# Optimization experiments

Hardware: AMD Instinct MI355X
Metric: run time of the kernel (lower is better)

Reference implementation:

```python
import jax, jax.numpy as jnp
import numpy as np
import math

BT, N, D, H = 16, 1024, 128, 8
HD = D // H


def setup_inputs() -> dict:
    key = jax.random.key(0)
    ks = jax.random.split(key, 12)
    s = 1.0 / math.sqrt(D)
    return {
        "x": jax.random.normal(ks[0], (BT, N, D), dtype=jnp.float32),
        "adj": jax.random.uniform(ks[1], (BT, N, N), dtype=jnp.float32),
        "Wq": jax.random.normal(ks[2], (D, D), dtype=jnp.float32) * s,
        "bq": jax.random.normal(ks[3], (D,), dtype=jnp.float32) * 0.01,
        "Wk": jax.random.normal(ks[4], (D, D), dtype=jnp.float32) * s,
        "bk": jax.random.normal(ks[5], (D,), dtype=jnp.float32) * 0.01,
        "Wv": jax.random.normal(ks[6], (D, D), dtype=jnp.float32) * s,
        "bv": jax.random.normal(ks[7], (D,), dtype=jnp.float32) * 0.01,
        "Wo": jax.random.normal(ks[8], (D, D), dtype=jnp.float32) * s,
        "bo": jax.random.normal(ks[9], (D,), dtype=jnp.float32) * 0.01,
    }


def reference(x, adj, Wq, bq, Wk, bk, Wv, bv, Wo, bo):
    bt, n, d = x.shape
    # projections (torch Linear: x @ W.T + b), split into heads -> (BT,H,N,HD)
    q = (x @ Wq.T + bq).reshape(bt, n, H, HD).transpose(0, 2, 1, 3)
    k = (x @ Wk.T + bk).reshape(bt, n, H, HD).transpose(0, 2, 1, 3)
    v = (x @ Wv.T + bv).reshape(bt, n, H, HD).transpose(0, 2, 1, 3)
    scores = jnp.einsum('bhnd,bhmd->bhnm', q, k) / math.sqrt(HD)  # (BT,H,N,N)
    mask = (adj == 0)[:, None, :, :]  # (BT,1,N,N)
    scores = jnp.where(mask, -jnp.inf, scores)
    attn = jax.nn.softmax(scores, axis=-1)
    attn = attn * adj[:, None, :, :]  # reweight by continuous causal strength
    attn = attn / (attn.sum(axis=-1, keepdims=True) + 1e-8)  # renormalize
    ctx = jnp.einsum('bhnm,bhmd->bhnd', attn, v)  # (BT,H,N,HD)
    ctx = ctx.transpose(0, 2, 1, 3).reshape(bt, n, d)
    return ctx @ Wo.T + bo
```

## Files before the change

kernel.cpp:

```cpp
#include <hip/hip_runtime.h>
#include <hip/hip_bf16.h>

#define BTC 16
#define NC 1024
#define DC 128
#define HC 8
#define HDC 16

typedef __attribute__((ext_vector_type(8))) short bf16x8;
typedef __attribute__((ext_vector_type(4))) float f32x4;
typedef __attribute__((ext_vector_type(16))) float f32x16;
typedef __attribute__((ext_vector_type(4))) short short4v;

#if __has_builtin(__builtin_amdgcn_exp2f)
#define EXP2F(x) __builtin_amdgcn_exp2f(x)
#else
#define EXP2F(x) exp2f(x)
#endif

#define QSCALE 0.36067376022224085f

union PK2 { short4v s4; __hip_bfloat162 h2[2]; };
union PK8 { bf16x8 v; short s[8]; __hip_bfloat162 h2[4]; };

static __device__ inline short f2bf(float f) {
    unsigned u = __builtin_bit_cast(unsigned, f);
    u += 0x7fffu + ((u >> 16) & 1u);
    return (short)(u >> 16);
}

#define LDS_BARRIER()                                              \
    do {                                                           \
        asm volatile("s_waitcnt lgkmcnt(0)" ::: "memory");         \
        __builtin_amdgcn_s_barrier();                              \
        asm volatile("" ::: "memory");                             \
    } while (0)

__global__ __launch_bounds__(256)
void prep_kernel(const float* __restrict__ x,
                 const float* __restrict__ Wq, const float* __restrict__ Wk,
                 const float* __restrict__ Wv, const float* __restrict__ Wo,
                 short* __restrict__ xbf, short* __restrict__ Wbf)
{
    int gid  = blockIdx.x * 256 + threadIdx.x;
    int base = gid * 4;
    const float* src;
    short* dst;
    if (base < 2097152) {
        src = x + base; dst = xbf + base;
    } else {
        int idx = base - 2097152;
        int w   = idx >> 14;
        int off = idx & 16383;
        src = ((w == 0) ? Wq : (w == 1) ? Wk : (w == 2) ? Wv : Wo) + off;
        dst = Wbf + w * 16384 + off;
    }
    float4 v = *(const float4*)src;
    PK2 pk;
    pk.h2[0] = __float22bfloat162_rn(make_float2(v.x, v.y));
    pk.h2[1] = __float22bfloat162_rn(make_float2(v.z, v.w));
    *(short4v*)dst = pk.s4;
}

__global__ __launch_bounds__(256)
void proj_qkv(const short* __restrict__ xbf, const short* __restrict__ Wbf,
              const float* __restrict__ bq, const float* __restrict__ bk,
              const float* __restrict__ bv,
              short* __restrict__ qo, short* __restrict__ ko, short* __restrict__ vto)
{
    __shared__ short T[128 * 72];

    const int y = blockIdx.y;
    const short* W = Wbf + y * 16384;
    const float* bias = (y == 0) ? bq : (y == 1) ? bk : bv;
    const float scale = (y == 0) ? QSCALE : 1.0f;

    const int tid  = threadIdx.x;
    const int wave = tid >> 6;
    const int lane = tid & 63;
    const int l15  = lane & 15;
    const int quad = lane >> 4;
    const int rowA = blockIdx.x * 64 + wave * 16;

    f32x4 acc[8];
#pragma unroll
    for (int t = 0; t < 8; ++t) acc[t] = (f32x4){0.f, 0.f, 0.f, 0.f};

#pragma unroll
    for (int kk = 0; kk < DC; kk += 32) {
        bf16x8 Af = *(const bf16x8*)&xbf[(size_t)(rowA + l15) * DC + kk + quad * 8];
#pragma unroll
        for (int t = 0; t < 8; ++t) {
            bf16x8 Bf = *(const bf16x8*)&W[(t * 16 + l15) * DC + kk + quad * 8];
            acc[t] = __builtin_amdgcn_mfma_f32_16x16x32_bf16(Af, Bf, acc[t], 0, 0, 0);
        }
    }

    if (y == 2) {
#pragma unroll
        for (int t = 0; t < 8; ++t) {
            int c = t * 16 + l15;
            float b = bias[c];
            PK2 pk;
            pk.h2[0] = __float22bfloat162_rn(make_float2(acc[t][0] + b, acc[t][1] + b));
            pk.h2[1] = __float22bfloat162_rn(make_float2(acc[t][2] + b, acc[t][3] + b));
            *(short4v*)&T[c * 72 + wave * 16 + quad * 4] = pk.s4;
        }
        __syncthreads();
        const int bt = blockIdx.x >> 4;
        const int n0 = (blockIdx.x * 64) & 1023;
        const int chunk = tid & 7;
        const int dr    = tid >> 3;
#pragma unroll
        for (int rep = 0; rep < 4; ++rep) {
            int d = rep * 32 + dr;
            bf16x8 u = *(const bf16x8*)&T[d * 72 + chunk * 8];
            *(bf16x8*)&vto[((size_t)bt * DC + d) * NC + n0 + chunk * 8] = u;
        }
    } else {
        short* dst = (y == 0) ? qo : ko;
#pragma unroll
        for (int t = 0; t < 8; ++t) {
            int c  = t * 16 + l15;
            int hh = c >> 4, dd = c & 15;
            float b = bias[c];
#pragma unroll
            for (int r = 0; r < 4; ++r) {
                int row = rowA + quad * 4 + r;
                int btq = row >> 10, n = row & 1023;
                float val = (acc[t][r] + b) * scale;
                dst[(((size_t)btq * HC + hh) * NC + n) * HDC + dd] = f2bf(val);
            }
        }
    }
}

__global__ __launch_bounds__(256)
void proj_out(const short* __restrict__ cbf, const short* __restrict__ Wobf,
              const float* __restrict__ bo, float* __restrict__ out)
{
    const int tid  = threadIdx.x;
    const int wave = tid >> 6;
    const int lane = tid & 63;
    const int l15  = lane & 15;
    const int quad = lane >> 4;
    const int rowA = blockIdx.x * 64 + wave * 16;

    f32x4 acc[8];
#pragma unroll
    for (int t = 0; t < 8; ++t) acc[t] = (f32x4){0.f, 0.f, 0.f, 0.f};

#pragma unroll
    for (int kk = 0; kk < DC; kk += 32) {
        bf16x8 Af = *(const bf16x8*)&cbf[(size_t)(rowA + l15) * DC + kk + quad * 8];
#pragma unroll
        for (int t = 0; t < 8; ++t) {
            bf16x8 Bf = *(const bf16x8*)&Wobf[(t * 16 + l15) * DC + kk + quad * 8];
            acc[t] = __builtin_amdgcn_mfma_f32_16x16x32_bf16(Af, Bf, acc[t], 0, 0, 0);
        }
    }

#pragma unroll
    for (int t = 0; t < 8; ++t) {
        int c = t * 16 + l15;
        float b = bo[c];
#pragma unroll
        for (int r = 0; r < 4; ++r) {
            int row = rowA + quad * 4 + r;
            out[(size_t)row * DC + c] = acc[t][r] + b;
        }
    }
}

__global__ __launch_bounds__(512, 4)
void attn_kernel(const short* __restrict__ qh, const short* __restrict__ kh,
                 const short* __restrict__ vt, const float* __restrict__ adj,
                 short* __restrict__ cb)
{
    __shared__ float As[2][32 * 36];
    __shared__ short Ps[8][2][32 * 40];

    const int tid  = threadIdx.x;
    const int wave = tid >> 6;
    const int lane = tid & 63;
    const int l31  = lane & 31;
    const int hi   = lane >> 5;
    const int l15  = lane & 15;
    const int quad = lane >> 4;
    const int bt   = blockIdx.y;
    const int qt0  = blockIdx.x * 32;
    const int h    = wave;

    const size_t xb = (size_t)bt * NC * DC;
    const size_t hb = ((size_t)bt * HC + h) * NC;

    const short* kp = kh + hb * HDC + hi * 8;
    const short* vp = vt + ((size_t)bt * DC + h * HDC + l15) * NC;
    const int arow = tid >> 4;
    const int acol = (tid & 15) * 2;
    const float* aptr = adj + (size_t)bt * NC * NC + (size_t)(qt0 + arow) * NC + acol;

    float2 ar  = *(const float2*)aptr;
    bf16x8 Ak  = *(const bf16x8*)&kp[(size_t)l31 * HDC];
    bf16x8 Bv  = *(const bf16x8*)&vp[quad * 8];
    const bf16x8 Bq = *(const bf16x8*)&qh[(hb + qt0 + l31) * HDC + hi * 8];

    PK8 ones;
#pragma unroll
    for (int j = 0; j < 8; ++j) ones.s[j] = (short)0x3F80;

    f32x16 Z16;
#pragma unroll
    for (int i = 0; i < 16; ++i) Z16[i] = 0.f;

    f32x4 Cc[2], Cw[2];
#pragma unroll
    for (int s = 0; s < 2; ++s) {
        Cc[s] = (f32x4){0.f, 0.f, 0.f, 0.f};
        Cw[s] = (f32x4){0.f, 0.f, 0.f, 0.f};
    }

#define EXPTILE(Sv, abuf, Pc)                                                 \
    do {                                                                      \
        _Pragma("unroll")                                                     \
        for (int t = 0; t < 4; ++t) {                                         \
            float4 a4 = *(const float4*)&As[abuf][l31 * 36 + t * 8 + hi * 4]; \
            float p0 = EXP2F(Sv[4 * t + 0]) * a4.x;                           \
            float p1 = EXP2F(Sv[4 * t + 1]) * a4.y;                           \
            float p2 = EXP2F(Sv[4 * t + 2]) * a4.z;                           \
            float p3 = EXP2F(Sv[4 * t + 3]) * a4.w;                           \
            PK2 pk;                                                           \
            pk.h2[0] = __float22bfloat162_rn(make_float2(p0, p1));            \
            pk.h2[1] = __float22bfloat162_rn(make_float2(p2, p3));            \
            *(short4v*)&Pc[l31 * 40 + t * 8 + hi * 4] = pk.s4;                \
        }                                                                     \
    } while (0)

    {
        *(float2*)&As[0][arow * 36 + acol] = ar;
        float2 arn = *(const float2*)(aptr + 32);
        LDS_BARRIER();
        bf16x8 Akn = *(const bf16x8*)&kp[(size_t)(32 + l31) * HDC];
        bf16x8 Bvn = *(const bf16x8*)&vp[32 + quad * 8];
        f32x16 S = __builtin_amdgcn_mfma_f32_32x32x16_bf16(Ak, Bq, Z16, 0, 0, 0);
        short* Pc = &Ps[wave][0][0];
        EXPTILE(S, 0, Pc);
        Ak = Akn; Bv = Bvn; ar = arn;
    }
    bf16x8 Bvp = Bv;

    Bvp = *(const bf16x8*)&vp[quad * 8];

#pragma unroll 2
    for (int it = 1; it < 32; ++it) {
        const int jt  = it * 32;
        const int cur = it & 1, prv = cur ^ 1;

        *(float2*)&As[cur][arow * 36 + acol] = ar;
        float2 arn = *(const float2*)(aptr + ((jt + 32) & (NC - 1)));
        LDS_BARRIER();

        const int nj = (jt + 32) & (NC - 1);
        bf16x8 Akn = *(const bf16x8*)&kp[(size_t)(nj + l31) * HDC];
        bf16x8 Bvn = *(const bf16x8*)&vp[nj + quad * 8];

        const short* Pr = &Ps[wave][prv][0];
        bf16x8 Ap0 = *(const bf16x8*)&Pr[l15 * 40 + quad * 8];
        bf16x8 Ap1 = *(const bf16x8*)&Pr[(16 + l15) * 40 + quad * 8];

        f32x16 S = __builtin_amdgcn_mfma_f32_32x32x16_bf16(Ak, Bq, Z16, 0, 0, 0);
        short* Pc = &Ps[wave][cur][0];
        EXPTILE(S, cur, Pc);

        __builtin_amdgcn_s_setprio(1);
        Cc[0] = __builtin_amdgcn_mfma_f32_16x16x32_bf16(Ap0, Bvp, Cc[0], 0, 0, 0);
        Cw[0] = __builtin_amdgcn_mfma_f32_16x16x32_bf16(Ap0, ones.v, Cw[0], 0, 0, 0);
        Cc[1] = __builtin_amdgcn_mfma_f32_16x16x32_bf16(Ap1, Bvp, Cc[1], 0, 0, 0);
        Cw[1] = __builtin_amdgcn_mfma_f32_16x16x32_bf16(Ap1, ones.v, Cw[1], 0, 0, 0);
        __builtin_amdgcn_s_setprio(0);

        Ak = Akn; Bvp = Bv; Bv = Bvn; ar = arn;
    }

    {
        const short* Pr = &Ps[wave][1][0];
        bf16x8 Ap0 = *(const bf16x8*)&Pr[l15 * 40 + quad * 8];
        bf16x8 Ap1 = *(const bf16x8*)&Pr[(16 + l15) * 40 + quad * 8];
        Cc[0] = __builtin_amdgcn_mfma_f32_16x16x32_bf16(Ap0, Bvp, Cc[0], 0, 0, 0);
        Cw[0] = __builtin_amdgcn_mfma_f32_16x16x32_bf16(Ap0, ones.v, Cw[0], 0, 0, 0);
        Cc[1] = __builtin_amdgcn_mfma_f32_16x16x32_bf16(Ap1, Bvp, Cc[1], 0, 0, 0);
        Cw[1] = __builtin_amdgcn_mfma_f32_16x16x32_bf16(Ap1, ones.v, Cw[1], 0, 0, 0);
    }

#pragma unroll
    for (int s = 0; s < 2; ++s)
#pragma unroll
        for (int r = 0; r < 4; ++r) {
            float den = Cw[s][r];
            float rcp = den > 0.f ? 1.f / den : 0.f;
            int row = qt0 + s * 16 + quad * 4 + r;
            cb[xb + (size_t)row * DC + h * HDC + l15] = f2bf(Cc[s][r] * rcp);
        }
#undef EXPTILE
}

extern "C" void kernel_launch(void* const* d_in, const int* in_sizes, int n_in,
                              void* d_out, int out_size, void* d_ws, size_t ws_size,
                              hipStream_t stream)
{
    const float* x   = (const float*)d_in[0];
    const float* adj = (const float*)d_in[1];
    const float* Wq  = (const float*)d_in[2];
    const float* bq  = (const float*)d_in[3];
    const float* Wk  = (const float*)d_in[4];
    const float* bk  = (const float*)d_in[5];
    const float* Wv  = (const float*)d_in[6];
    const float* bv  = (const float*)d_in[7];
    const float* Wo  = (const float*)d_in[8];
    const float* bo  = (const float*)d_in[9];
    float* out = (float*)d_out;

    const size_t tok = (size_t)BTC * NC * DC;
    short* xbf  = (short*)d_ws;
    short* Wbf  = xbf  + tok;
    short* qbuf = Wbf  + 65536;
    short* kbuf = qbuf + tok;
    short* vt   = kbuf + tok;
    short* cbuf = vt   + tok;

    prep_kernel<<<2112, 256, 0, stream>>>(x, Wq, Wk, Wv, Wo, xbf, Wbf);

    dim3 pgrid(256, 3);
    proj_qkv<<<pgrid, 256, 0, stream>>>(xbf, Wbf, bq, bk, bv, qbuf, kbuf, vt);

    dim3 agrid(32, 16);
    attn_kernel<<<agrid, 512, 0, stream>>>(qbuf, kbuf, vt, adj, cbuf);

    proj_out<<<256, 256, 0, stream>>>(cbuf, Wbf + 3 * 16384, bo, out);
}
```

Measured before the change: 167.0 us.

## Shrink attention query tile to 16 rows with 16x16 MFMAs and swizzled LDS

```diff
diff --git a/kernel.cpp b/kernel.cpp
--- a/kernel.cpp
+++ b/kernel.cpp
@@ -9,7 +9,6 @@
 
 typedef __attribute__((ext_vector_type(8))) short bf16x8;
 typedef __attribute__((ext_vector_type(4))) float f32x4;
-typedef __attribute__((ext_vector_type(16))) float f32x16;
 typedef __attribute__((ext_vector_type(4))) short short4v;
 
 #if __has_builtin(__builtin_amdgcn_exp2f)
@@ -27,6 +26,18 @@
     unsigned u = __builtin_bit_cast(unsigned, f);
     u += 0x7fffu + ((u >> 16) & 1u);
     return (short)(u >> 16);
+}
+
+static __device__ inline f32x4 qkmfma(short4v a, short4v b, f32x4 c) {
+#if __has_builtin(__builtin_amdgcn_mfma_f32_16x16x16bf16_1k)
+    return __builtin_amdgcn_mfma_f32_16x16x16bf16_1k(a, b, c, 0, 0, 0);
+#elif __has_builtin(__builtin_amdgcn_mfma_f32_16x16x16_bf16)
+    return __builtin_amdgcn_mfma_f32_16x16x16_bf16(a, b, c, 0, 0, 0);
+#else
+    bf16x8 a8 = {a[0], a[1], a[2], a[3], 0, 0, 0, 0};
+    bf16x8 b8 = {b[0], b[1], b[2], b[3], 0, 0, 0, 0};
+    return __builtin_amdgcn_mfma_f32_16x16x32_bf16(a8, b8, c, 0, 0, 0);
+#endif
 }
 
 #define LDS_BARRIER()                                              \
@@ -111,11 +122,14 @@
         const int n0 = (blockIdx.x * 64) & 1023;
         const int chunk = tid & 7;
         const int dr    = tid >> 3;
+        const int tb    = (chunk >> 2) * 32 + (chunk & 3) * 4;
 #pragma unroll
         for (int rep = 0; rep < 4; ++rep) {
             int d = rep * 32 + dr;
-            bf16x8 u = *(const bf16x8*)&T[d * 72 + chunk * 8];
-            *(bf16x8*)&vto[((size_t)bt * DC + d) * NC + n0 + chunk * 8] = u;
+            PK8 u;
+            *(short4v*)&u.s[0] = *(const short4v*)&T[d * 72 + tb];
+            *(short4v*)&u.s[4] = *(const short4v*)&T[d * 72 + tb + 16];
+            *(bf16x8*)&vto[((size_t)bt * DC + d) * NC + n0 + chunk * 8] = u.v;
         }
     } else {
         short* dst = (y == 0) ? qo : ko;
@@ -172,136 +186,127 @@
     }
 }
 
-__global__ __launch_bounds__(512, 4)
+__global__ __launch_bounds__(512, 6)
 void attn_kernel(const short* __restrict__ qh, const short* __restrict__ kh,
                  const short* __restrict__ vt, const float* __restrict__ adj,
                  short* __restrict__ cb)
 {
-    __shared__ float As[2][32 * 36];
-    __shared__ short Ps[8][2][32 * 40];
+    __shared__ float As[2][16 * 32];
+    __shared__ short Ps[8][2][16 * 64];
 
     const int tid  = threadIdx.x;
     const int wave = tid >> 6;
     const int lane = tid & 63;
-    const int l31  = lane & 31;
-    const int hi   = lane >> 5;
     const int l15  = lane & 15;
     const int quad = lane >> 4;
     const int bt   = blockIdx.y;
-    const int qt0  = blockIdx.x * 32;
+    const int qt0  = blockIdx.x * 16;
     const int h    = wave;
 
     const size_t xb = (size_t)bt * NC * DC;
     const size_t hb = ((size_t)bt * HC + h) * NC;
 
-    const short* kp = kh + hb * HDC + hi * 8;
+    const short* kp2 = kh + (hb + l15) * HDC + quad * 4;
     const short* vp = vt + ((size_t)bt * DC + h * HDC + l15) * NC;
-    const int arow = tid >> 4;
-    const int acol = (tid & 15) * 2;
+    const short4v Bq = *(const short4v*)&qh[(hb + qt0 + l15) * HDC + quad * 4];
+
+    const int arow = tid >> 5;
+    const int acol = tid & 31;
     const float* aptr = adj + (size_t)bt * NC * NC + (size_t)(qt0 + arow) * NC + acol;
-
-    float2 ar  = *(const float2*)aptr;
-    bf16x8 Ak  = *(const bf16x8*)&kp[(size_t)l31 * HDC];
-    bf16x8 Bv  = *(const bf16x8*)&vp[quad * 8];
-    const bf16x8 Bq = *(const bf16x8*)&qh[(hb + qt0 + l31) * HDC + hi * 8];
-
-    PK8 ones;
-#pragma unroll
-    for (int j = 0; j < 8; ++j) ones.s[j] = (short)0x3F80;
-
-    f32x16 Z16;
-#pragma unroll
-    for (int i = 0; i < 16; ++i) Z16[i] = 0.f;
-
-    f32x4 Cc[2], Cw[2];
-#pragma unroll
-    for (int s = 0; s < 2; ++s) {
-        Cc[s] = (f32x4){0.f, 0.f, 0.f, 0.f};
-        Cw[s] = (f32x4){0.f, 0.f, 0.f, 0.f};
-    }
-
-#define EXPTILE(Sv, abuf, Pc)                                                 \
+    const unsigned awb = (unsigned)((arow * 128 + acol * 4) ^ ((arow & 7) << 4));
+
+    const unsigned arb0 = (unsigned)((l15 * 128 + quad * 16) ^ ((l15 & 7) << 4));
+    const unsigned arb1 = arb0 ^ 64;
+    const unsigned pwb = (unsigned)((l15 * 128 + quad * 16) ^ ((l15 & 7) << 4));
+
+    const f32x4 z4 = (f32x4){0.f, 0.f, 0.f, 0.f};
+    f32x4 Cc = z4;
+    float wsum = 0.f;
+
+    char* AsCur = (char*)&As[0][0];
+    char* AsNxt = (char*)&As[1][0];
+    char* Pa = (char*)&Ps[wave][0][0];
+    char* Pb = (char*)&Ps[wave][1][0];
+
+    float ar = aptr[0];
+
+#define EXPBLK(ASB, PDST)                                                     \
     do {                                                                      \
-        _Pragma("unroll")                                                     \
-        for (int t = 0; t < 4; ++t) {                                         \
-            float4 a4 = *(const float4*)&As[abuf][l31 * 36 + t * 8 + hi * 4]; \
-            float p0 = EXP2F(Sv[4 * t + 0]) * a4.x;                           \
-            float p1 = EXP2F(Sv[4 * t + 1]) * a4.y;                           \
-            float p2 = EXP2F(Sv[4 * t + 2]) * a4.z;                           \
-            float p3 = EXP2F(Sv[4 * t + 3]) * a4.w;                           \
-            PK2 pk;                                                           \
-            pk.h2[0] = __float22bfloat162_rn(make_float2(p0, p1));            \
-            pk.h2[1] = __float22bfloat162_rn(make_float2(p2, p3));            \
-            *(short4v*)&Pc[l31 * 40 + t * 8 + hi * 4] = pk.s4;                \
-        }                                                                     \
+        float4 a40 = *(const float4*)((ASB) + arb0);                          \
+        float4 a41 = *(const float4*)((ASB) + arb1);                          \
+        float p0 = EXP2F(S0[0]) * a40.x;                                      \
+        float p1 = EXP2F(S0[1]) * a40.y;                                      \
+        float p2 = EXP2F(S0[2]) * a40.z;                                      \
+        float p3 = EXP2F(S0[3]) * a40.w;                                      \
+        float p4 = EXP2F(S1[0]) * a41.x;                                      \
+        float p5 = EXP2F(S1[1]) * a41.y;                                      \
+        float p6 = EXP2F(S1[2]) * a41.z;                                      \
+        float p7 = EXP2F(S1[3]) * a41.w;                                      \
+        wsum += ((p0 + p1) + (p2 + p3)) + ((p4 + p5) + (p6 + p7));            \
+        PK8 pk;                                                               \
+        pk.h2[0] = __float22bfloat162_rn(make_float2(p0, p1));                \
+        pk.h2[1] = __float22bfloat162_rn(make_float2(p2, p3));                \
+        pk.h2[2] = __float22bfloat162_rn(make_float2(p4, p5));                \
+        pk.h2[3] = __float22bfloat162_rn(make_float2(p6, p7));                \
+        *(bf16x8*)((PDST) + pwb) = pk.v;                                      \
     } while (0)
 
     {
-        *(float2*)&As[0][arow * 36 + acol] = ar;
-        float2 arn = *(const float2*)(aptr + 32);
+        *(float*)(AsCur + awb) = ar;
+        ar = aptr[32];
         LDS_BARRIER();
-        bf16x8 Akn = *(const bf16x8*)&kp[(size_t)(32 + l31) * HDC];
-        bf16x8 Bvn = *(const bf16x8*)&vp[32 + quad * 8];
-        f32x16 S = __builtin_amdgcn_mfma_f32_32x32x16_bf16(Ak, Bq, Z16, 0, 0, 0);
-        short* Pc = &Ps[wave][0][0];
-        EXPTILE(S, 0, Pc);
-        Ak = Akn; Bv = Bvn; ar = arn;
-    }
-    bf16x8 Bvp = Bv;
-
-    Bvp = *(const bf16x8*)&vp[quad * 8];
+        short4v Ak0 = *(const short4v*)&kp2[0];
+        short4v Ak1 = *(const short4v*)&kp2[16 * HDC];
+        f32x4 S0 = qkmfma(Ak0, Bq, z4);
+        f32x4 S1 = qkmfma(Ak1, Bq, z4);
+        EXPBLK(AsCur, Pa);
+        { char* t = Pa; Pa = Pb; Pb = t; }
+        { char* t = AsCur; AsCur = AsNxt; AsNxt = t; }
+    }
 
 #pragma unroll 2
     for (int it = 1; it < 32; ++it) {
-        const int jt  = it * 32;
-        const int cur = it & 1, prv = cur ^ 1;
-
-        *(float2*)&As[cur][arow * 36 + acol] = ar;
-        float2 arn = *(const float2*)(aptr + ((jt + 32) & (NC - 1)));
+        const int jt = it * 32;
+
+        *(float*)(AsCur + awb) = ar;
+        ar = aptr[(jt + 32) & (NC - 1)];
         LDS_BARRIER();
 
-        const int nj = (jt + 32) & (NC - 1);
-        bf16x8 Akn = *(const bf16x8*)&kp[(size_t)(nj + l31) * HDC];
-        bf16x8 Bvn = *(const bf16x8*)&vp[nj + quad * 8];
-
-        const short* Pr = &Ps[wave][prv][0];
-        bf16x8 Ap0 = *(const bf16x8*)&Pr[l15 * 40 + quad * 8];
-        bf16x8 Ap1 = *(const bf16x8*)&Pr[(16 + l15) * 40 + quad * 8];
-
-        f32x16 S = __builtin_amdgcn_mfma_f32_32x32x16_bf16(Ak, Bq, Z16, 0, 0, 0);
-        short* Pc = &Ps[wave][cur][0];
-        EXPTILE(S, cur, Pc);
+        short4v Ak0 = *(const short4v*)&kp2[jt * HDC];
+        short4v Ak1 = *(const short4v*)&kp2[(jt + 16) * HDC];
+        bf16x8  Bv  = *(const bf16x8*)&vp[jt - 32 + quad * 8];
+        bf16x8  Ap  = *(const bf16x8*)(Pb + pwb);
+
+        f32x4 S0 = qkmfma(Ak0, Bq, z4);
+        f32x4 S1 = qkmfma(Ak1, Bq, z4);
+        EXPBLK(AsCur, Pa);
+        __builtin_amdgcn_wave_barrier();
 
         __builtin_amdgcn_s_setprio(1);
-        Cc[0] = __builtin_amdgcn_mfma_f32_16x16x32_bf16(Ap0, Bvp, Cc[0], 0, 0, 0);
-        Cw[0] = __builtin_amdgcn_mfma_f32_16x16x32_bf16(Ap0, ones.v, Cw[0], 0, 0, 0);
-        Cc[1] = __builtin_amdgcn_mfma_f32_16x16x32_bf16(Ap1, Bvp, Cc[1], 0, 0, 0);
-        Cw[1] = __builtin_amdgcn_mfma_f32_16x16x32_bf16(Ap1, ones.v, Cw[1], 0, 0, 0);
+        Cc = __builtin_amdgcn_mfma_f32_16x16x32_bf16(Ap, Bv, Cc, 0, 0, 0);
         __builtin_amdgcn_s_setprio(0);
 
-        Ak = Akn; Bvp = Bv; Bv = Bvn; ar = arn;
+        { char* t = Pa; Pa = Pb; Pb = t; }
+        { char* t = AsCur; AsCur = AsNxt; AsNxt = t; }
     }
 
     {
-        const short* Pr = &Ps[wave][1][0];
-        bf16x8 Ap0 = *(const bf16x8*)&Pr[l15 * 40 + quad * 8];
-        bf16x8 Ap1 = *(const bf16x8*)&Pr[(16 + l15) * 40 + quad * 8];
-        Cc[0] = __builtin_amdgcn_mfma_f32_16x16x32_bf16(Ap0, Bvp, Cc[0], 0, 0, 0);
-        Cw[0] = __builtin_amdgcn_mfma_f32_16x16x32_bf16(Ap0, ones.v, Cw[0], 0, 0, 0);
-        Cc[1] = __builtin_amdgcn_mfma_f32_16x16x32_bf16(Ap1, Bvp, Cc[1], 0, 0, 0);
-        Cw[1] = __builtin_amdgcn_mfma_f32_16x16x32_bf16(Ap1, ones.v, Cw[1], 0, 0, 0);
-    }
-
-#pragma unroll
-    for (int s = 0; s < 2; ++s)
-#pragma unroll
-        for (int r = 0; r < 4; ++r) {
-            float den = Cw[s][r];
-            float rcp = den > 0.f ? 1.f / den : 0.f;
-            int row = qt0 + s * 16 + quad * 4 + r;
-            cb[xb + (size_t)row * DC + h * HDC + l15] = f2bf(Cc[s][r] * rcp);
-        }
-#undef EXPTILE
+        bf16x8 Bv = *(const bf16x8*)&vp[992 + quad * 8];
+        bf16x8 Ap = *(const bf16x8*)(Pb + pwb);
+        Cc = __builtin_amdgcn_mfma_f32_16x16x32_bf16(Ap, Bv, Cc, 0, 0, 0);
+    }
+
+    wsum += __shfl_xor(wsum, 16);
+    wsum += __shfl_xor(wsum, 32);
+
+#pragma unroll
+    for (int r = 0; r < 4; ++r) {
+        float den = __shfl(wsum, quad * 4 + r);
+        float rcp = den > 0.f ? 1.f / den : 0.f;
+        int row = qt0 + quad * 4 + r;
+        cb[xb + (size_t)row * DC + h * HDC + l15] = f2bf(Cc[r] * rcp);
+    }
+#undef EXPBLK
 }
 
 extern "C" void kernel_launch(void* const* d_in, const int* in_sizes, int n_in,
@@ -333,7 +338,7 @@
     dim3 pgrid(256, 3);
     proj_qkv<<<pgrid, 256, 0, stream>>>(xbf, Wbf, bq, bk, bv, qbuf, kbuf, vt);
 
-    dim3 agrid(32, 16);
+    dim3 agrid(64, 16);
     attn_kernel<<<agrid, 512, 0, stream>>>(qbuf, kbuf, vt, adj, cbuf);
 
     proj_out<<<256, 256, 0, stream>>>(cbuf, Wbf + 3 * 16384, bo, out);
```

New measurement: 205.1 us. +22.8%, slower.

## Split attention heads across two blocks and re-pipeline adj staging and P tiles

Applied to the files above, without the earlier changes.

```diff
diff --git a/kernel.cpp b/kernel.cpp
--- a/kernel.cpp
+++ b/kernel.cpp
@@ -172,13 +172,13 @@
     }
 }
 
-__global__ __launch_bounds__(512, 4)
+__global__ __launch_bounds__(256, 4)
 void attn_kernel(const short* __restrict__ qh, const short* __restrict__ kh,
                  const short* __restrict__ vt, const float* __restrict__ adj,
                  short* __restrict__ cb)
 {
     __shared__ float As[2][32 * 36];
-    __shared__ short Ps[8][2][32 * 40];
+    __shared__ short Ps[4][2][32 * 40];
 
     const int tid  = threadIdx.x;
     const int wave = tid >> 6;
@@ -189,21 +189,19 @@
     const int quad = lane >> 4;
     const int bt   = blockIdx.y;
     const int qt0  = blockIdx.x * 32;
-    const int h    = wave;
+    const int h    = blockIdx.z * 4 + wave;
 
     const size_t xb = (size_t)bt * NC * DC;
     const size_t hb = ((size_t)bt * HC + h) * NC;
 
-    const short* kp = kh + hb * HDC + hi * 8;
+    const short* kp = kh + (hb + l31) * HDC + hi * 8;
     const short* vp = vt + ((size_t)bt * DC + h * HDC + l15) * NC;
-    const int arow = tid >> 4;
-    const int acol = (tid & 15) * 2;
+    const bf16x8 Bq = *(const bf16x8*)&qh[(hb + qt0 + l31) * HDC + hi * 8];
+
+    const int arow = tid >> 3;
+    const int acol = (tid & 7) * 4;
     const float* aptr = adj + (size_t)bt * NC * NC + (size_t)(qt0 + arow) * NC + acol;
-
-    float2 ar  = *(const float2*)aptr;
-    bf16x8 Ak  = *(const bf16x8*)&kp[(size_t)l31 * HDC];
-    bf16x8 Bv  = *(const bf16x8*)&vp[quad * 8];
-    const bf16x8 Bq = *(const bf16x8*)&qh[(hb + qt0 + l31) * HDC + hi * 8];
+    const int awoff = arow * 36 + acol;
 
     PK8 ones;
 #pragma unroll
@@ -220,57 +218,76 @@
         Cw[s] = (f32x4){0.f, 0.f, 0.f, 0.f};
     }
 
-#define EXPTILE(Sv, abuf, Pc)                                                 \
+    short* Pa = &Ps[wave][0][0];
+    short* Pb = &Ps[wave][1][0];
+
+    float4 ar = *(const float4*)aptr;
+    bf16x8 Ak = *(const bf16x8*)&kp[0];
+    bf16x8 Bv = *(const bf16x8*)&vp[quad * 8];
+    bf16x8 Bvp;
+
+#define EXPTILE(ASB, PDST)                                                    \
     do {                                                                      \
-        _Pragma("unroll")                                                     \
-        for (int t = 0; t < 4; ++t) {                                         \
-            float4 a4 = *(const float4*)&As[abuf][l31 * 36 + t * 8 + hi * 4]; \
-            float p0 = EXP2F(Sv[4 * t + 0]) * a4.x;                           \
-            float p1 = EXP2F(Sv[4 * t + 1]) * a4.y;                           \
-            float p2 = EXP2F(Sv[4 * t + 2]) * a4.z;                           \
-            float p3 = EXP2F(Sv[4 * t + 3]) * a4.w;                           \
-            PK2 pk;                                                           \
-            pk.h2[0] = __float22bfloat162_rn(make_float2(p0, p1));            \
-            pk.h2[1] = __float22bfloat162_rn(make_float2(p2, p3));            \
-            *(short4v*)&Pc[l31 * 40 + t * 8 + hi * 4] = pk.s4;                \
-        }                                                                     \
+        const float* asb = (ASB) + l31 * 36 + hi * 4;                         \
+        float4 a0 = *(const float4*)&asb[0];                                  \
+        float4 a1 = *(const float4*)&asb[8];                                  \
+        float4 a2 = *(const float4*)&asb[16];                                 \
+        float4 a3 = *(const float4*)&asb[24];                                 \
+        short* pd = (PDST) + l31 * 40 + hi * 4;                               \
+        PK2 pk;                                                               \
+        pk.h2[0] = __float22bfloat162_rn(                                     \
+            make_float2(EXP2F(S[0]) * a0.x, EXP2F(S[1]) * a0.y));             \
+        pk.h2[1] = __float22bfloat162_rn(                                     \
+            make_float2(EXP2F(S[2]) * a0.z, EXP2F(S[3]) * a0.w));             \
+        *(short4v*)&pd[0] = pk.s4;                                            \
+        pk.h2[0] = __float22bfloat162_rn(                                     \
+            make_float2(EXP2F(S[4]) * a1.x, EXP2F(S[5]) * a1.y));             \
+        pk.h2[1] = __float22bfloat162_rn(                                     \
+            make_float2(EXP2F(S[6]) * a1.z, EXP2F(S[7]) * a1.w));             \
+        *(short4v*)&pd[8] = pk.s4;                                            \
+        pk.h2[0] = __float22bfloat162_rn(                                     \
+            make_float2(EXP2F(S[8]) * a2.x, EXP2F(S[9]) * a2.y));             \
+        pk.h2[1] = __float22bfloat162_rn(                                     \
+            make_float2(EXP2F(S[10]) * a2.z, EXP2F(S[11]) * a2.w));           \
+        *(short4v*)&pd[16] = pk.s4;                                           \
+        pk.h2[0] = __float22bfloat162_rn(                                     \
+            make_float2(EXP2F(S[12]) * a3.x, EXP2F(S[13]) * a3.y));           \
+        pk.h2[1] = __float22bfloat162_rn(                                     \
+            make_float2(EXP2F(S[14]) * a3.z, EXP2F(S[15]) * a3.w));           \
+        *(short4v*)&pd[24] = pk.s4;                                           \
     } while (0)
 
+    *(float4*)((char*)&As[0][0] + 0 + awoff * 4) = ar;
+    ar = *(const float4*)(aptr + 32);
+    LDS_BARRIER();
+
     {
-        *(float2*)&As[0][arow * 36 + acol] = ar;
-        float2 arn = *(const float2*)(aptr + 32);
-        LDS_BARRIER();
-        bf16x8 Akn = *(const bf16x8*)&kp[(size_t)(32 + l31) * HDC];
+        *(float4*)&As[1][awoff] = ar;
+        ar = *(const float4*)(aptr + 64);
+        bf16x8 Akn = *(const bf16x8*)&kp[32 * HDC];
         bf16x8 Bvn = *(const bf16x8*)&vp[32 + quad * 8];
         f32x16 S = __builtin_amdgcn_mfma_f32_32x32x16_bf16(Ak, Bq, Z16, 0, 0, 0);
-        short* Pc = &Ps[wave][0][0];
-        EXPTILE(S, 0, Pc);
-        Ak = Akn; Bv = Bvn; ar = arn;
-    }
-    bf16x8 Bvp = Bv;
-
-    Bvp = *(const bf16x8*)&vp[quad * 8];
+        EXPTILE(&As[0][0], Pa);
+        LDS_BARRIER();
+        { short* t = Pa; Pa = Pb; Pb = t; }
+        Ak = Akn; Bvp = Bv; Bv = Bvn;
+    }
 
 #pragma unroll 2
     for (int it = 1; it < 32; ++it) {
         const int jt  = it * 32;
-        const int cur = it & 1, prv = cur ^ 1;
-
-        *(float2*)&As[cur][arow * 36 + acol] = ar;
-        float2 arn = *(const float2*)(aptr + ((jt + 32) & (NC - 1)));
-        LDS_BARRIER();
-
-        const int nj = (jt + 32) & (NC - 1);
-        bf16x8 Akn = *(const bf16x8*)&kp[(size_t)(nj + l31) * HDC];
-        bf16x8 Bvn = *(const bf16x8*)&vp[nj + quad * 8];
-
-        const short* Pr = &Ps[wave][prv][0];
-        bf16x8 Ap0 = *(const bf16x8*)&Pr[l15 * 40 + quad * 8];
-        bf16x8 Ap1 = *(const bf16x8*)&Pr[(16 + l15) * 40 + quad * 8];
+        const int cur = it & 1;
+
+        *(float4*)&As[cur ^ 1][awoff] = ar;
+        ar = *(const float4*)(aptr + ((jt + 64) & (NC - 1)));
+
+        bf16x8 Akn = *(const bf16x8*)&kp[((jt + 32) & (NC - 1)) * HDC];
+        bf16x8 Bvn = *(const bf16x8*)&vp[((jt + 32) & (NC - 1)) + quad * 8];
+
+        bf16x8 Ap0 = *(const bf16x8*)&Pb[l15 * 40 + quad * 8];
+        bf16x8 Ap1 = *(const bf16x8*)&Pb[(16 + l15) * 40 + quad * 8];
 
         f32x16 S = __builtin_amdgcn_mfma_f32_32x32x16_bf16(Ak, Bq, Z16, 0, 0, 0);
-        short* Pc = &Ps[wave][cur][0];
-        EXPTILE(S, cur, Pc);
 
         __builtin_amdgcn_s_setprio(1);
         Cc[0] = __builtin_amdgcn_mfma_f32_16x16x32_bf16(Ap0, Bvp, Cc[0], 0, 0, 0);
@@ -279,13 +296,16 @@
         Cw[1] = __builtin_amdgcn_mfma_f32_16x16x32_bf16(Ap1, ones.v, Cw[1], 0, 0, 0);
         __builtin_amdgcn_s_setprio(0);
 
-        Ak = Akn; Bvp = Bv; Bv = Bvn; ar = arn;
+        EXPTILE(&As[cur][0], Pa);
+        LDS_BARRIER();
+
+        { short* t = Pa; Pa = Pb; Pb = t; }
+        Ak = Akn; Bvp = Bv; Bv = Bvn;
     }
 
     {
-        const short* Pr = &Ps[wave][1][0];
-        bf16x8 Ap0 = *(const bf16x8*)&Pr[l15 * 40 + quad * 8];
-        bf16x8 Ap1 = *(const bf16x8*)&Pr[(16 + l15) * 40 + quad * 8];
+        bf16x8 Ap0 = *(const bf16x8*)&Pb[l15 * 40 + quad * 8];
+        bf16x8 Ap1 = *(const bf16x8*)&Pb[(16 + l15) * 40 + quad * 8];
         Cc[0] = __builtin_amdgcn_mfma_f32_16x16x32_bf16(Ap0, Bvp, Cc[0], 0, 0, 0);
         Cw[0] = __builtin_amdgcn_mfma_f32_16x16x32_bf16(Ap0, ones.v, Cw[0], 0, 0, 0);
         Cc[1] = __builtin_amdgcn_mfma_f32_16x16x32_bf16(Ap1, Bvp, Cc[1], 0, 0, 0);
@@ -333,8 +353,8 @@
     dim3 pgrid(256, 3);
     proj_qkv<<<pgrid, 256, 0, stream>>>(xbf, Wbf, bq, bk, bv, qbuf, kbuf, vt);
 
-    dim3 agrid(32, 16);
-    attn_kernel<<<agrid, 512, 0, stream>>>(qbuf, kbuf, vt, adj, cbuf);
+    dim3 agrid(32, 16, 2);
+    attn_kernel<<<agrid, 256, 0, stream>>>(qbuf, kbuf, vt, adj, cbuf);
 
     proj_out<<<256, 256, 0, stream>>>(cbuf, Wbf + 3 * 16384, bo, out);
 }
```

After: 174.6 us. 1.05x slower.
